# Optimization experiments

Measured on AMD Instinct MI355X. Metric: run time of the kernel, lower is better.

## Reference

```python
import jax, jax.numpy as jnp
import numpy as np
import math

HIDDEN = 2048
N_Q = 16
N_KV = 8
HEAD_DIM = 128
THETA = 10000.0
RANK = 8
ALPHA = 16
LORA_SCALING = ALPHA / RANK  # 2.0
SCALING = 1.0 / math.sqrt(HEAD_DIM)


def setup_inputs() -> dict:
    key = jax.random.key(0)
    ks = jax.random.split(key, 14)
    B, S = 2, 2048
    std = 0.02
    inp = {
        "x": jax.random.normal(ks[0], (B, S, HIDDEN), dtype=jnp.float32),
        # nn.Linear weights: [out_features, in_features]
        "Wq": jax.random.normal(ks[1], (N_Q * HEAD_DIM, HIDDEN), dtype=jnp.float32) * std,
        "Wk": jax.random.normal(ks[2], (N_KV * HEAD_DIM, HIDDEN), dtype=jnp.float32) * std,
        "Wv": jax.random.normal(ks[3], (N_KV * HEAD_DIM, HIDDEN), dtype=jnp.float32) * std,
        "Wo": jax.random.normal(ks[4], (HIDDEN, N_Q * HEAD_DIM), dtype=jnp.float32) * std,
        "qA": jax.random.normal(ks[5], (RANK, HIDDEN), dtype=jnp.float32) * std,
        "qB": jax.random.normal(ks[6], (N_Q * HEAD_DIM, RANK), dtype=jnp.float32) * std,
        "kA": jax.random.normal(ks[7], (RANK, HIDDEN), dtype=jnp.float32) * std,
        "kB": jax.random.normal(ks[8], (N_KV * HEAD_DIM, RANK), dtype=jnp.float32) * std,
        "vA": jax.random.normal(ks[9], (RANK, HIDDEN), dtype=jnp.float32) * std,
        "vB": jax.random.normal(ks[10], (N_KV * HEAD_DIM, RANK), dtype=jnp.float32) * std,
        "oA": jax.random.normal(ks[11], (RANK, N_Q * HEAD_DIM), dtype=jnp.float32) * std,
        "oB": jax.random.normal(ks[12], (HIDDEN, RANK), dtype=jnp.float32) * std,
    }
    return inp


def _rope_cos_sin(seq_len, dtype):
    inv_freq = 1.0 / (THETA ** (jnp.arange(0, HEAD_DIM, 2, dtype=jnp.float32) / HEAD_DIM))
    t = jnp.arange(seq_len, dtype=jnp.float32)
    freqs = t[:, None] * inv_freq[None, :]  # [S, D/2]
    return jnp.cos(freqs).astype(dtype), jnp.sin(freqs).astype(dtype)


def _apply_rope(x, cos, sin):
    # x: [B, H, S, D]; interleaved real/imag pairs on last dim
    xr = x[..., ::2]
    xi = x[..., 1::2]
    rr = xr * cos - xi * sin
    ri = xr * sin + xi * cos
    return jnp.stack([rr, ri], axis=-1).reshape(x.shape)


def _forward(x, Wq, Wk, Wv, Wo, qA, qB, kA, kB, vA, vB, oA, oB):
    B, S, H = x.shape
    # base projections + LoRA (low-rank path kept factored: (x @ A^T) @ B^T)
    q = x @ Wq.T + ((x @ qA.T) @ qB.T) * LORA_SCALING  # [B,S,NQ*D]
    k = x @ Wk.T + ((x @ kA.T) @ kB.T) * LORA_SCALING  # [B,S,NKV*D]
    v = x @ Wv.T + ((x @ vA.T) @ vB.T) * LORA_SCALING
    q = q.reshape(B, S, N_Q, HEAD_DIM).transpose(0, 2, 1, 3)   # [B,NQ,S,D]
    k = k.reshape(B, S, N_KV, HEAD_DIM).transpose(0, 2, 1, 3)  # [B,NKV,S,D]
    v = v.reshape(B, S, N_KV, HEAD_DIM).transpose(0, 2, 1, 3)
    cos, sin = _rope_cos_sin(S, x.dtype)  # [S, D/2] each
    q = _apply_rope(q, cos, sin)
    k = _apply_rope(k, cos, sin)
    if N_Q != N_KV:
        rep = N_Q // N_KV
        k = jnp.repeat(k, rep, axis=1)  # [B,NQ,S,D]
        v = jnp.repeat(v, rep, axis=1)
    scores = jnp.einsum('bhqd,bhkd->bhqk', q, k) * SCALING
    causal = jnp.tril(jnp.ones((S, S), dtype=bool))
    scores = jnp.where(causal, scores, -jnp.inf)
    attn = jax.nn.softmax(scores, axis=-1).astype(v.dtype)
    out = jnp.einsum('bhqk,bhkd->bhqd', attn, v)  # [B,NQ,S,D]
    out = out.transpose(0, 2, 1, 3).reshape(B, S, N_Q * HEAD_DIM)
    return out @ Wo.T + ((out @ oA.T) @ oB.T) * LORA_SCALING


def reference(x, Wq, Wk, Wv, Wo, qA, qB, kA, kB, vA, vB, oA, oB):
    return _forward(x, Wq, Wk, Wv, Wo, qA, qB, kA, kB, vA, vB, oA, oB)
```

## Files before the change

kernel.cpp:

```cpp
#include <hip/hip_runtime.h>
#include <hip/hip_bf16.h>
#include <cmath>

#define HIDDEN 2048
#define SEQ 2048
#define BATCH 2
#define NQ 16
#define NKV 8
#define HD 128
#define RANKL 8
#define LORA_SCALE 2.0f
#define INV_SQRT_D 0.08838834764831845f
#define LOG2E 1.4426950408889634f
#define SM_SCALE (INV_SQRT_D * LOG2E)

typedef unsigned short ushort_t;
typedef __bf16 bf16x8 __attribute__((ext_vector_type(8)));
typedef float f32x4 __attribute__((ext_vector_type(4)));

static __device__ __forceinline__ ushort_t f2bf(float f) {
    __hip_bfloat16 h = __float2bfloat16(f);
    return *(ushort_t*)&h;
}
static __device__ __forceinline__ float bf2f(ushort_t u) {
    unsigned int v = ((unsigned int)u) << 16;
    return __builtin_bit_cast(float, v);
}
static __device__ __forceinline__ void gload_lds16(const ushort_t* g, ushort_t* l) {
    __builtin_amdgcn_global_load_lds(
        (const __attribute__((address_space(1))) unsigned int*)g,
        (__attribute__((address_space(3))) unsigned int*)l, 16, 0, 0);
}

__global__ __launch_bounds__(256) void lora_cast_x(
    const float* __restrict__ X, ushort_t* __restrict__ Xbf,
    const float* __restrict__ qA, const float* __restrict__ kA,
    const float* __restrict__ vA,
    float* __restrict__ oq, float* __restrict__ ok, float* __restrict__ ov)
{
    int m = blockIdx.x;
    int t = threadIdx.x;
    int c0 = t * 8;
    const float* xr = X + (size_t)m * HIDDEN + c0;
    float4 a = *(const float4*)xr;
    float4 b = *(const float4*)(xr + 4);
    float xv[8] = {a.x, a.y, a.z, a.w, b.x, b.y, b.z, b.w};
    uint4 o;
    o.x = (unsigned int)f2bf(xv[0]) | ((unsigned int)f2bf(xv[1]) << 16);
    o.y = (unsigned int)f2bf(xv[2]) | ((unsigned int)f2bf(xv[3]) << 16);
    o.z = (unsigned int)f2bf(xv[4]) | ((unsigned int)f2bf(xv[5]) << 16);
    o.w = (unsigned int)f2bf(xv[6]) | ((unsigned int)f2bf(xv[7]) << 16);
    *(uint4*)(Xbf + (size_t)m * HIDDEN + c0) = o;

    float p[3][RANKL];
#pragma unroll
    for (int w = 0; w < 3; w++)
#pragma unroll
        for (int r = 0; r < RANKL; r++) p[w][r] = 0.f;
    const float* Aw[3] = {qA, kA, vA};
#pragma unroll
    for (int e = 0; e < 8; e++) {
        float x8 = xv[e];
#pragma unroll
        for (int w = 0; w < 3; w++)
#pragma unroll
            for (int r = 0; r < RANKL; r++)
                p[w][r] += x8 * Aw[w][r * HIDDEN + c0 + e];
    }
#pragma unroll
    for (int w = 0; w < 3; w++)
#pragma unroll
        for (int r = 0; r < RANKL; r++) {
            float v = p[w][r];
            v += __shfl_xor(v, 32); v += __shfl_xor(v, 16);
            v += __shfl_xor(v, 8);  v += __shfl_xor(v, 4);
            v += __shfl_xor(v, 2);  v += __shfl_xor(v, 1);
            p[w][r] = v;
        }
    __shared__ float wred[4][3][RANKL];
    int wave = t >> 6, lane = t & 63;
    if (lane == 0) {
#pragma unroll
        for (int w = 0; w < 3; w++)
#pragma unroll
            for (int r = 0; r < RANKL; r++) wred[wave][w][r] = p[w][r];
    }
    __syncthreads();
    if (t < 3 * RANKL) {
        int w = t / RANKL, r = t % RANKL;
        float s = wred[0][w][r] + wred[1][w][r] + wred[2][w][r] + wred[3][w][r];
        float* dst = (w == 0) ? oq : (w == 1) ? ok : ov;
        dst[(size_t)m * RANKL + r] = s;
    }
}

__global__ __launch_bounds__(256) void lora_xa_bf16(
    const ushort_t* __restrict__ X, const float* __restrict__ Aw,
    float* __restrict__ out, int K)
{
    int m = blockIdx.x;
    int t = threadIdx.x;
    const ushort_t* xr = X + (size_t)m * K;
    float p[RANKL];
#pragma unroll
    for (int r = 0; r < RANKL; r++) p[r] = 0.f;
    for (int c = t; c < K; c += 256) {
        float xv = bf2f(xr[c]);
#pragma unroll
        for (int r = 0; r < RANKL; r++) p[r] += xv * Aw[r * K + c];
    }
#pragma unroll
    for (int r = 0; r < RANKL; r++) {
        float v = p[r];
        v += __shfl_xor(v, 32); v += __shfl_xor(v, 16);
        v += __shfl_xor(v, 8);  v += __shfl_xor(v, 4);
        v += __shfl_xor(v, 2);  v += __shfl_xor(v, 1);
        p[r] = v;
    }
    __shared__ float wred[4][RANKL];
    int wave = t >> 6, lane = t & 63;
    if (lane == 0) {
#pragma unroll
        for (int r = 0; r < RANKL; r++) wred[wave][r] = p[r];
    }
    __syncthreads();
    if (t < RANKL) {
        out[(size_t)m * RANKL + t] =
            wred[0][t] + wred[1][t] + wred[2][t] + wred[3][t];
    }
}

__global__ __launch_bounds__(256) void cast_weights(
    const float* __restrict__ Wq, const float* __restrict__ Wk,
    const float* __restrict__ Wv, const float* __restrict__ Wo,
    ushort_t* __restrict__ Wqb, ushort_t* __restrict__ Wkb,
    ushort_t* __restrict__ Wvb, ushort_t* __restrict__ Wob)
{
    size_t i = (size_t)blockIdx.x * 256 + threadIdx.x;
    const float* src; ushort_t* dst; size_t j;
    if (i < 524288)       { src = Wq; dst = Wqb; j = i; }
    else if (i < 786432)  { src = Wk; dst = Wkb; j = i - 524288; }
    else if (i < 1048576) { src = Wv; dst = Wvb; j = i - 786432; }
    else                  { src = Wo; dst = Wob; j = i - 1048576; }
    const float4* p = (const float4*)src + j * 2;
    float4 a = p[0], b = p[1];
    uint4 o;
    o.x = (unsigned int)f2bf(a.x) | ((unsigned int)f2bf(a.y) << 16);
    o.y = (unsigned int)f2bf(a.z) | ((unsigned int)f2bf(a.w) << 16);
    o.z = (unsigned int)f2bf(b.x) | ((unsigned int)f2bf(b.y) << 16);
    o.w = (unsigned int)f2bf(b.z) | ((unsigned int)f2bf(b.w) << 16);
    *(uint4*)(dst + j * 8) = o;
}

static __device__ __forceinline__ void gemm_core(
    const ushort_t* __restrict__ A, const ushort_t* __restrict__ B,
    void* __restrict__ Cout, int N, int K, int bm, int bn,
    const float* __restrict__ xa, const float* __restrict__ LB,
    float lscale, int out_bf16, ushort_t* As, ushort_t* Bs)
{
    const int t = threadIdx.x;
    const int lane = t & 63;
    const int w = t >> 6;
    const int quad = lane >> 4;
    const int c = lane & 15;

    const int wm = (w & 1) * 64;
    const int wn = (w >> 1) * 64;

    f32x4 acc[4][4];
#pragma unroll
    for (int i = 0; i < 4; i++)
#pragma unroll
        for (int j = 0; j < 4; j++) acc[i][j] = (f32x4){0.f, 0.f, 0.f, 0.f};

    const int p0 = w * 64 + lane;
    const int p1 = 256 + w * 64 + lane;
    const int r0 = p0 >> 2, g0 = (p0 & 3) ^ ((p0 >> 3) & 3);
    const int r1 = p1 >> 2, g1 = (p1 & 3) ^ ((p1 >> 3) & 3);
    const ushort_t* gA0 = A + (size_t)(bm + r0) * K + g0 * 8;
    const ushort_t* gA1 = A + (size_t)(bm + r1) * K + g1 * 8;
    const ushort_t* gB0 = B + (size_t)(bn + r0) * K + g0 * 8;
    const ushort_t* gB1 = B + (size_t)(bn + r1) * K + g1 * 8;
    ushort_t* lA0 = As + (size_t)(w * 64) * 8;
    ushort_t* lA1 = As + (size_t)(256 + w * 64) * 8;
    ushort_t* lB0 = Bs + (size_t)(w * 64) * 8;
    ushort_t* lB1 = Bs + (size_t)(256 + w * 64) * 8;

    const int csw = quad ^ ((c >> 1) & 3);

    for (int k0 = 0; k0 < K; k0 += 32) {
        __syncthreads();
        gload_lds16(gA0 + k0, lA0);
        gload_lds16(gA1 + k0, lA1);
        gload_lds16(gB0 + k0, lB0);
        gload_lds16(gB1 + k0, lB1);
        __syncthreads();

        bf16x8 af[4], bfr[4];
#pragma unroll
        for (int mt = 0; mt < 4; mt++)
            af[mt] = *(const bf16x8*)&As[((wm + mt * 16 + c) * 4 + csw) * 8];
#pragma unroll
        for (int nt = 0; nt < 4; nt++)
            bfr[nt] = *(const bf16x8*)&Bs[((wn + nt * 16 + c) * 4 + csw) * 8];
#pragma unroll
        for (int mt = 0; mt < 4; mt++)
#pragma unroll
            for (int nt = 0; nt < 4; nt++)
                acc[mt][nt] = __builtin_amdgcn_mfma_f32_16x16x32_bf16(
                    af[mt], bfr[nt], acc[mt][nt], 0, 0, 0);
    }

    float lb[4][RANKL];
#pragma unroll
    for (int nt = 0; nt < 4; nt++) {
        int col = bn + wn + nt * 16 + c;
        float4 u = *(const float4*)&LB[(size_t)col * RANKL];
        float4 v = *(const float4*)&LB[(size_t)col * RANKL + 4];
        lb[nt][0] = u.x; lb[nt][1] = u.y; lb[nt][2] = u.z; lb[nt][3] = u.w;
        lb[nt][4] = v.x; lb[nt][5] = v.y; lb[nt][6] = v.z; lb[nt][7] = v.w;
    }
#pragma unroll
    for (int mt = 0; mt < 4; mt++) {
        float la[4][RANKL];
#pragma unroll
        for (int r = 0; r < 4; r++) {
            int row = bm + wm + mt * 16 + quad * 4 + r;
            float4 u = *(const float4*)&xa[(size_t)row * RANKL];
            float4 v = *(const float4*)&xa[(size_t)row * RANKL + 4];
            la[r][0] = u.x; la[r][1] = u.y; la[r][2] = u.z; la[r][3] = u.w;
            la[r][4] = v.x; la[r][5] = v.y; la[r][6] = v.z; la[r][7] = v.w;
        }
#pragma unroll
        for (int nt = 0; nt < 4; nt++) {
#pragma unroll
            for (int r = 0; r < 4; r++) {
                float s = 0.f;
#pragma unroll
                for (int k = 0; k < RANKL; k++) s += la[r][k] * lb[nt][k];
                float val = acc[mt][nt][r] + lscale * s;
                size_t row = bm + wm + mt * 16 + quad * 4 + r;
                size_t col = bn + wn + nt * 16 + c;
                if (out_bf16)
                    ((ushort_t*)Cout)[row * N + col] = f2bf(val);
                else
                    ((float*)Cout)[row * N + col] = val;
            }
        }
    }
}

__global__ __launch_bounds__(256) void gemm_qkv(
    const ushort_t* __restrict__ A,
    const ushort_t* __restrict__ Wqb, const ushort_t* __restrict__ Wkb,
    const ushort_t* __restrict__ Wvb,
    ushort_t* __restrict__ q_lin, ushort_t* __restrict__ k_lin,
    ushort_t* __restrict__ v_lin,
    const float* __restrict__ xa_q, const float* __restrict__ xa_k,
    const float* __restrict__ xa_v,
    const float* __restrict__ qB, const float* __restrict__ kB,
    const float* __restrict__ vB)
{
    __shared__ ushort_t As[128 * 32];
    __shared__ ushort_t Bs[128 * 32];
    int bc = blockIdx.y;
    const ushort_t* B; ushort_t* Cout; const float* xa; const float* LB;
    int N, bn;
    if (bc < 16)      { B = Wqb; Cout = q_lin; xa = xa_q; LB = qB; N = 2048; bn = bc * 128; }
    else if (bc < 24) { B = Wkb; Cout = k_lin; xa = xa_k; LB = kB; N = 1024; bn = (bc - 16) * 128; }
    else              { B = Wvb; Cout = v_lin; xa = xa_v; LB = vB; N = 1024; bn = (bc - 24) * 128; }
    gemm_core(A, B, Cout, N, HIDDEN, blockIdx.x * 128, bn, xa, LB,
              LORA_SCALE, 1, As, Bs);
}

__global__ __launch_bounds__(256) void gemm_wo(
    const ushort_t* __restrict__ A, const ushort_t* __restrict__ Wob,
    float* __restrict__ out, const float* __restrict__ xa_o,
    const float* __restrict__ oB)
{
    __shared__ ushort_t As[128 * 32];
    __shared__ ushort_t Bs[128 * 32];
    gemm_core(A, Wob, out, HIDDEN, NQ * HD, blockIdx.x * 128, blockIdx.y * 128,
              xa_o, oB, LORA_SCALE, 0, As, Bs);
}

__global__ __launch_bounds__(256) void rope_qk(
    const ushort_t* __restrict__ qlin, const ushort_t* __restrict__ klin,
    ushort_t* __restrict__ qb, ushort_t* __restrict__ kb)
{
    int bs = blockIdx.x;
    int s = bs & (SEQ - 1);
    int b = bs >> 11;
    int t = threadIdx.x;
    int p = t & 63;
    float inv = exp2f(-(float)p * 0.20762050593046f);
    float ang = (float)s * inv;
    float cc = cosf(ang), si = sinf(ang);
#pragma unroll
    for (int j = 0; j < 6; j++) {
        int item = t + 256 * j;
        int hh = item >> 6;
        unsigned int pk;
        ushort_t* dst;
        if (hh < NQ) {
            pk = *(const unsigned int*)&qlin[(size_t)bs * (NQ * HD) + hh * HD + 2 * p];
            dst = qb + (((size_t)(b * NQ + hh) * SEQ) + s) * HD + 2 * p;
        } else {
            int kh = hh - NQ;
            pk = *(const unsigned int*)&klin[(size_t)bs * (NKV * HD) + kh * HD + 2 * p];
            dst = kb + (((size_t)(b * NKV + kh) * SEQ) + s) * HD + 2 * p;
        }
        float xr = bf2f((ushort_t)(pk & 0xffff));
        float xi = bf2f((ushort_t)(pk >> 16));
        float rr = xr * cc - xi * si;
        float ri = xr * si + xi * cc;
        *(unsigned int*)dst = ((unsigned int)f2bf(ri) << 16) | f2bf(rr);
    }
}

__global__ __launch_bounds__(256) void v_transpose(
    const ushort_t* __restrict__ vlin, ushort_t* __restrict__ Vt)
{
    int bk = blockIdx.x;
    int b = bk >> 3, kvh = bk & 7;
    int s0 = blockIdx.y * 64, d0 = blockIdx.z * 64;
    __shared__ ushort_t tile[64 * 72];
    int t = threadIdx.x;
#pragma unroll
    for (int i = 0; i < 2; i++) {
        int id = t + 256 * i;
        int r = id >> 3, cc = id & 7;
        uint4 v = *(const uint4*)&vlin[(size_t)(b * SEQ + s0 + r) * (NKV * HD)
                                       + kvh * HD + d0 + cc * 8];
        *(uint4*)&tile[r * 72 + cc * 8] = v;
    }
    __syncthreads();
#pragma unroll
    for (int i = 0; i < 2; i++) {
        int id = t + 256 * i;
        int dr = id >> 3, sc = id & 7;
        ushort_t tmp[8];
#pragma unroll
        for (int e = 0; e < 8; e++) tmp[e] = tile[(sc * 8 + e) * 72 + dr];
        *(uint4*)&Vt[((size_t)(b * NKV + kvh) * HD + d0 + dr) * SEQ + s0 + sc * 8]
            = *(uint4*)tmp;
    }
}

__global__ __launch_bounds__(256, 2) void attn_mfma3(
    const ushort_t* __restrict__ Q, const ushort_t* __restrict__ K,
    const ushort_t* __restrict__ V, ushort_t* __restrict__ O)
{
    __shared__ ushort_t Ks[2][64 * 128];
    __shared__ ushort_t Vs[2][128 * 64];
    __shared__ ushort_t Psh[4][16 * 68];

    const int t = threadIdx.x;
    const int lane = t & 63;
    const int w = t >> 6;
    const int quad = lane >> 4;
    const int c = lane & 15;
    const int q4 = quad * 4;
    const int c7 = c & 7;

    const int head = blockIdx.x >> 4;
    const int a = blockIdx.x & 15;
    const int h = head & (NQ - 1);
    const int b = head >> 4;
    const int kvh = b * NKV + (h >> 1);

    const ushort_t* Kg = K + (size_t)kvh * SEQ * HD;
    const ushort_t* Vg = V + (size_t)kvh * HD * SEQ;

    const ushort_t* gK[4]; const ushort_t* gV[4];
    int lo[4];
#pragma unroll
    for (int i = 0; i < 4; i++) {
        int cid = t + 256 * i;
        int kr = cid >> 4, kc = cid & 15;
        gK[i] = Kg + (size_t)kr * HD + ((kc ^ (kr & 7)) * 8);
        int vd = cid >> 3, vc = cid & 7;
        gV[i] = Vg + (size_t)vd * SEQ + ((vc ^ (vd & 7)) * 8);
        lo[i] = (i * 256 + (t & ~63)) * 8;
    }

#pragma unroll 1
    for (int half = 0; half < 2; half++) {
        const int qt = half ? (31 - a) : a;
        const int qb0 = qt * 64;
        const int myrow = qb0 + w * 16;

        const ushort_t* Qg = Q + ((size_t)head * SEQ + myrow + c) * HD;
        bf16x8 qf[4];
#pragma unroll
        for (int ch = 0; ch < 4; ch++)
            qf[ch] = *(const bf16x8*)(Qg + ch * 32 + quad * 8);

        f32x4 o[8];
#pragma unroll
        for (int i = 0; i < 8; i++) o[i] = (f32x4){0.f, 0.f, 0.f, 0.f};
        float lp[4] = {0.f, 0.f, 0.f, 0.f};

        const int ntiles = qt + 1;

#pragma unroll
        for (int i = 0; i < 4; i++) gload_lds16(gK[i], &Ks[0][lo[i]]);
#pragma unroll
        for (int i = 0; i < 4; i++) gload_lds16(gV[i], &Vs[0][lo[i]]);
        __syncthreads();

        for (int tile = 0; tile < ntiles; ++tile) {
            const int cur = tile & 1;
            if (tile + 1 < ntiles) {
                const int j1 = (tile + 1) * 64;
#pragma unroll
                for (int i = 0; i < 4; i++)
                    gload_lds16(gK[i] + (size_t)j1 * HD, &Ks[cur ^ 1][lo[i]]);
#pragma unroll
                for (int i = 0; i < 4; i++)
                    gload_lds16(gV[i] + j1, &Vs[cur ^ 1][lo[i]]);
            }

            f32x4 s[4];
#pragma unroll
            for (int tt = 0; tt < 4; tt++) s[tt] = (f32x4){0.f, 0.f, 0.f, 0.f};
#pragma unroll
            for (int tt = 0; tt < 4; tt++) {
                const int krow = tt * 16 + c;
#pragma unroll
                for (int ch = 0; ch < 4; ch++) {
                    bf16x8 kf = *(const bf16x8*)
                        &Ks[cur][krow * 128 + (((ch * 4 + quad) ^ c7) * 8)];
                    s[tt] = __builtin_amdgcn_mfma_f32_16x16x32_bf16(
                        qf[ch], kf, s[tt], 0, 0, 0);
                }
            }

            const bool diag = (tile == qt);
            const int j0 = tile * 64;
#pragma unroll
            for (int r = 0; r < 4; r++) {
                const int row_g = myrow + q4 + r;
#pragma unroll
                for (int tt = 0; tt < 4; tt++) {
                    float p = exp2f(s[tt][r] * SM_SCALE);
                    if (diag && (j0 + tt * 16 + c > row_g)) p = 0.f;
                    Psh[w][(q4 + r) * 68 + tt * 16 + c] = f2bf(p);
                    lp[r] += p;
                }
            }

            bf16x8 pf[2];
#pragma unroll
            for (int ch = 0; ch < 2; ch++) {
                int base = c * 68 + ch * 32 + quad * 8;
                uint2 aa = *(const uint2*)&Psh[w][base];
                uint2 bb = *(const uint2*)&Psh[w][base + 4];
                uint4 u; u.x = aa.x; u.y = aa.y; u.z = bb.x; u.w = bb.y;
                pf[ch] = __builtin_bit_cast(bf16x8, u);
            }

#pragma unroll
            for (int dt = 0; dt < 8; dt++) {
                const int vrow = dt * 16 + c;
#pragma unroll
                for (int ch = 0; ch < 2; ch++) {
                    bf16x8 vf = *(const bf16x8*)
                        &Vs[cur][vrow * 64 + (((ch * 4 + quad) ^ c7) * 8)];
                    o[dt] = __builtin_amdgcn_mfma_f32_16x16x32_bf16(
                        pf[ch], vf, o[dt], 0, 0, 0);
                }
            }
            __syncthreads();
        }

        float inv[4];
#pragma unroll
        for (int r = 0; r < 4; r++) {
            float v = lp[r];
            v += __shfl_xor(v, 1);
            v += __shfl_xor(v, 2);
            v += __shfl_xor(v, 4);
            v += __shfl_xor(v, 8);
            inv[r] = 1.f / v;
        }
        size_t base = ((size_t)b * SEQ + myrow + q4) * (NQ * HD) + h * HD + c;
#pragma unroll
        for (int r = 0; r < 4; r++)
#pragma unroll
            for (int dt = 0; dt < 8; dt++)
                O[base + (size_t)r * (NQ * HD) + dt * 16] =
                    f2bf(o[dt][r] * inv[r]);
    }
}

extern "C" void kernel_launch(void* const* d_in, const int* in_sizes, int n_in,
                              void* d_out, int out_size, void* d_ws, size_t ws_size,
                              hipStream_t stream)
{
    const float* x  = (const float*)d_in[0];
    const float* Wq = (const float*)d_in[1];
    const float* Wk = (const float*)d_in[2];
    const float* Wv = (const float*)d_in[3];
    const float* Wo = (const float*)d_in[4];
    const float* qA = (const float*)d_in[5];
    const float* qB = (const float*)d_in[6];
    const float* kA = (const float*)d_in[7];
    const float* kB = (const float*)d_in[8];
    const float* vA = (const float*)d_in[9];
    const float* vB = (const float*)d_in[10];
    const float* oA = (const float*)d_in[11];
    const float* oB = (const float*)d_in[12];
    float* out = (float*)d_out;
    float* ws = (float*)d_ws;

    const int M = BATCH * SEQ;

    float* xa_q = ws;
    float* xa_k = ws + 32768;
    float* xa_v = ws + 65536;
    float* xa_o = ws + 98304;
    ushort_t* q_lin = (ushort_t*)(ws + 131072);
    ushort_t* k_lin = (ushort_t*)(ws + 4325376);
    ushort_t* v_lin = (ushort_t*)(ws + 6422528);
    ushort_t* qb    = (ushort_t*)(ws + 8519680);
    ushort_t* kb    = (ushort_t*)(ws + 12713984);
    ushort_t* vtb   = (ushort_t*)(ws + 14811136);
    ushort_t* xbf   = (ushort_t*)(ws + 16908288);
    ushort_t* Wqb   = (ushort_t*)(ws + 21102592);
    ushort_t* Wkb   = (ushort_t*)(ws + 23199744);
    ushort_t* Wvb   = (ushort_t*)(ws + 24248320);
    ushort_t* Wob   = (ushort_t*)(ws + 25296896);
    ushort_t* attn_out = q_lin;

    lora_cast_x<<<M, 256, 0, stream>>>(x, xbf, qA, kA, vA, xa_q, xa_k, xa_v);

    cast_weights<<<6144, 256, 0, stream>>>(Wq, Wk, Wv, Wo, Wqb, Wkb, Wvb, Wob);

    gemm_qkv<<<dim3(M / 128, 32), 256, 0, stream>>>(
        xbf, Wqb, Wkb, Wvb, q_lin, k_lin, v_lin,
        xa_q, xa_k, xa_v, qB, kB, vB);

    rope_qk<<<M, 256, 0, stream>>>(q_lin, k_lin, qb, kb);
    v_transpose<<<dim3(BATCH * NKV, SEQ / 64, HD / 64), 256, 0, stream>>>(v_lin, vtb);

    attn_mfma3<<<512, 256, 0, stream>>>(qb, kb, vtb, attn_out);

    lora_xa_bf16<<<M, 256, 0, stream>>>(attn_out, oA, xa_o, NQ * HD);
    gemm_wo<<<dim3(M / 128, HIDDEN / 128), 256, 0, stream>>>(
        attn_out, Wob, out, xa_o, oB);
}
```

Before: 420.9 us.

## Rewrite QKV GEMM with 256x256 tiles, async LDS loads and double buffering

Replaces the shared 128x128 GEMM core for the QKV projection with a dedicated 512-thread kernel using 256x256 output tiles and a K-step of 64. Global data goes directly to LDS through a double-buffered pipeline with staggered prefetch, an XOR-swizzled LDS layout and the 16x16x32 bf16 MFMA. The aim is more data reuse per tile and hiding global memory latency behind compute. The cost is higher register and LDS pressure, and a grid of only 16x16 blocks, which may leave some CUs idle.

```diff
diff --git a/kernel.cpp b/kernel.cpp
--- a/kernel.cpp
+++ b/kernel.cpp
@@ -250,7 +250,10 @@
     }
 }
 
-__global__ __launch_bounds__(256) void gemm_qkv(
+#define BKT 64
+#define NKT (HIDDEN / BKT)
+
+__global__ __launch_bounds__(512, 2) void gemm_qkv256(
     const ushort_t* __restrict__ A,
     const ushort_t* __restrict__ Wqb, const ushort_t* __restrict__ Wkb,
     const ushort_t* __restrict__ Wvb,
@@ -261,16 +264,156 @@
     const float* __restrict__ qB, const float* __restrict__ kB,
     const float* __restrict__ vB)
 {
-    __shared__ ushort_t As[128 * 32];
-    __shared__ ushort_t Bs[128 * 32];
-    int bc = blockIdx.y;
-    const ushort_t* B; ushort_t* Cout; const float* xa; const float* LB;
+    __shared__ __align__(16) ushort_t As[2][256 * BKT];
+    __shared__ __align__(16) ushort_t Bs[2][256 * BKT];
+
+    const int t = threadIdx.x;
+    const int lane = t & 63;
+    const int w = t >> 6;
+    const int wm = w >> 2;
+    const int wn = w & 3;
+    const int quad = lane >> 4;
+    const int c = lane & 15;
+    const int c7 = c & 7;
+
+    const int bc = blockIdx.y;
+    const ushort_t* Bmat; ushort_t* Cout; const float* xa; const float* LB;
     int N, bn;
-    if (bc < 16)      { B = Wqb; Cout = q_lin; xa = xa_q; LB = qB; N = 2048; bn = bc * 128; }
-    else if (bc < 24) { B = Wkb; Cout = k_lin; xa = xa_k; LB = kB; N = 1024; bn = (bc - 16) * 128; }
-    else              { B = Wvb; Cout = v_lin; xa = xa_v; LB = vB; N = 1024; bn = (bc - 24) * 128; }
-    gemm_core(A, B, Cout, N, HIDDEN, blockIdx.x * 128, bn, xa, LB,
-              LORA_SCALE, 1, As, Bs);
+    if (bc < 8)       { Bmat = Wqb; Cout = q_lin; xa = xa_q; LB = qB; N = 2048; bn = bc * 256; }
+    else if (bc < 12) { Bmat = Wkb; Cout = k_lin; xa = xa_k; LB = kB; N = 1024; bn = (bc - 8) * 256; }
+    else              { Bmat = Wvb; Cout = v_lin; xa = xa_v; LB = vB; N = 1024; bn = (bc - 12) * 256; }
+    const int bm = blockIdx.x * 256;
+
+    const int r8  = lane >> 3;
+    const int ksl = (lane & 7) ^ r8;
+    const int ga  = wn;
+    const int bh  = wn >> 1;
+    const int gb  = wm * 2 + (wn & 1);
+
+    const ushort_t* gAb = A    + (size_t)(bm + wm * 128 + ga * 8 + r8) * HIDDEN + ksl * 8;
+    const ushort_t* gBb = Bmat + (size_t)(bn + bh * 128 + gb * 8 + r8) * HIDDEN + ksl * 8;
+    const int lAoff = (wm * 128 + ga * 8) * BKT;
+    const int lBoff = (bh * 128 + gb * 8) * BKT;
+
+#pragma unroll
+    for (int j = 0; j < 4; j++) {
+        gload_lds16(gAb + (size_t)j * 32 * HIDDEN, &As[0][lAoff + j * 32 * BKT]);
+        gload_lds16(gBb + (size_t)j * 32 * HIDDEN, &Bs[0][lBoff + j * 32 * BKT]);
+    }
+#pragma unroll
+    for (int j = 0; j < 3; j++) {
+        gload_lds16(gAb + (size_t)j * 32 * HIDDEN + BKT, &As[1][lAoff + j * 32 * BKT]);
+        gload_lds16(gBb + (size_t)j * 32 * HIDDEN + BKT, &Bs[1][lBoff + j * 32 * BKT]);
+    }
+
+    f32x4 acc[8][4];
+#pragma unroll
+    for (int i = 0; i < 8; i++)
+#pragma unroll
+        for (int j = 0; j < 4; j++) acc[i][j] = (f32x4){0.f, 0.f, 0.f, 0.f};
+
+#pragma unroll 1
+    for (int T = 0; T < NKT; ++T) {
+        const int cur = T & 1;
+        const ushort_t* cA = As[cur];
+        const ushort_t* cB = Bs[cur];
+        bf16x8 bfr[4][2];
+
+#pragma unroll
+        for (int q = 0; q < 4; ++q) {
+            if (q == 0) {
+                asm volatile("s_waitcnt vmcnt(6)" ::: "memory");
+            }
+            __builtin_amdgcn_sched_barrier(0);
+            __builtin_amdgcn_s_barrier();
+            __builtin_amdgcn_sched_barrier(0);
+
+            bf16x8 af[2][2];
+#pragma unroll
+            for (int m2 = 0; m2 < 2; ++m2) {
+                const int row = wm * 128 + (q * 2 + m2) * 16 + c;
+#pragma unroll
+                for (int kh = 0; kh < 2; ++kh)
+                    af[m2][kh] = *(const bf16x8*)
+                        &cA[row * BKT + (((kh * 4 + quad) ^ c7) * 8)];
+            }
+            if (q == 0) {
+#pragma unroll
+                for (int nt = 0; nt < 4; ++nt) {
+                    const int rowb = wn * 64 + nt * 16 + c;
+#pragma unroll
+                    for (int kh = 0; kh < 2; ++kh)
+                        bfr[nt][kh] = *(const bf16x8*)
+                            &cB[rowb * BKT + (((kh * 4 + quad) ^ c7) * 8)];
+                }
+            }
+
+            if (q == 0) {
+                const int tl = T + 1;
+                if (tl < NKT) {
+                    gload_lds16(gAb + (size_t)3 * 32 * HIDDEN + (size_t)tl * BKT,
+                                &As[cur ^ 1][lAoff + 3 * 32 * BKT]);
+                    gload_lds16(gBb + (size_t)3 * 32 * HIDDEN + (size_t)tl * BKT,
+                                &Bs[cur ^ 1][lBoff + 3 * 32 * BKT]);
+                }
+            } else {
+                const int tl = T + 2;
+                if (tl < NKT) {
+                    const int j = q - 1;
+                    gload_lds16(gAb + (size_t)j * 32 * HIDDEN + (size_t)tl * BKT,
+                                &As[cur][lAoff + j * 32 * BKT]);
+                    gload_lds16(gBb + (size_t)j * 32 * HIDDEN + (size_t)tl * BKT,
+                                &Bs[cur][lBoff + j * 32 * BKT]);
+                }
+            }
+
+            __builtin_amdgcn_s_setprio(1);
+#pragma unroll
+            for (int m2 = 0; m2 < 2; ++m2)
+#pragma unroll
+                for (int nt = 0; nt < 4; ++nt)
+#pragma unroll
+                    for (int kh = 0; kh < 2; ++kh)
+                        acc[q * 2 + m2][nt] = __builtin_amdgcn_mfma_f32_16x16x32_bf16(
+                            af[m2][kh], bfr[nt][kh], acc[q * 2 + m2][nt], 0, 0, 0);
+            __builtin_amdgcn_s_setprio(0);
+        }
+    }
+
+    float lb[4][RANKL];
+#pragma unroll
+    for (int nt = 0; nt < 4; nt++) {
+        int col = bn + wn * 64 + nt * 16 + c;
+        float4 u = *(const float4*)&LB[(size_t)col * RANKL];
+        float4 v = *(const float4*)&LB[(size_t)col * RANKL + 4];
+        lb[nt][0] = u.x; lb[nt][1] = u.y; lb[nt][2] = u.z; lb[nt][3] = u.w;
+        lb[nt][4] = v.x; lb[nt][5] = v.y; lb[nt][6] = v.z; lb[nt][7] = v.w;
+    }
+#pragma unroll
+    for (int mt = 0; mt < 8; mt++) {
+        float la[4][RANKL];
+#pragma unroll
+        for (int r = 0; r < 4; r++) {
+            int row = bm + wm * 128 + mt * 16 + quad * 4 + r;
+            float4 u = *(const float4*)&xa[(size_t)row * RANKL];
+            float4 v = *(const float4*)&xa[(size_t)row * RANKL + 4];
+            la[r][0] = u.x; la[r][1] = u.y; la[r][2] = u.z; la[r][3] = u.w;
+            la[r][4] = v.x; la[r][5] = v.y; la[r][6] = v.z; la[r][7] = v.w;
+        }
+#pragma unroll
+        for (int nt = 0; nt < 4; nt++) {
+#pragma unroll
+            for (int r = 0; r < 4; r++) {
+                float s = 0.f;
+#pragma unroll
+                for (int k = 0; k < RANKL; k++) s += la[r][k] * lb[nt][k];
+                float val = acc[mt][nt][r] + LORA_SCALE * s;
+                size_t row = bm + wm * 128 + mt * 16 + quad * 4 + r;
+                size_t col = bn + wn * 64 + nt * 16 + c;
+                Cout[row * N + col] = f2bf(val);
+            }
+        }
+    }
 }
 
 __global__ __launch_bounds__(256) void gemm_wo(
@@ -537,7 +680,7 @@
 
     cast_weights<<<6144, 256, 0, stream>>>(Wq, Wk, Wv, Wo, Wqb, Wkb, Wvb, Wob);
 
-    gemm_qkv<<<dim3(M / 128, 32), 256, 0, stream>>>(
+    gemm_qkv256<<<dim3(M / 256, 16), 512, 0, stream>>>(
         xbf, Wqb, Wkb, Wvb, q_lin, k_lin, v_lin,
         xa_q, xa_k, xa_v, qB, kB, vB);
 
```

After: 393.2 us. 6.6% less time.
